# Kernel tuning notes

Hardware: AMD Instinct MI355X
Metric: run time of the kernel (lower is better)

Reference implementation:

```python
import jax, jax.numpy as jnp
import numpy as np

D_MODEL = 96
D_INNER = 2 * D_MODEL          # expand=2
D_STATE = 16
D_CONV = 4
DT_RANK = 6                    # ceil(96/16)


def setup_inputs() -> dict:
    key = jax.random.key(0)
    ks = jax.random.split(key, 12)
    B, C, H, W = 4, D_MODEL, 64, 64
    # dt_proj bias init (inverse-softplus of dt sampled log-uniform in [1e-3, 1e-1])
    dtv = jnp.exp(jax.random.uniform(ks[7], (D_INNER,), jnp.float32)
                  * (np.log(0.1) - np.log(0.001)) + np.log(0.001))
    dtv = jnp.clip(dtv, 1e-4, None)
    dt_proj_b = dtv + jnp.log(-jnp.expm1(-dtv))
    dt_std = DT_RANK ** -0.5
    return {
        "x": jax.random.normal(ks[0], (B, C, H, W), jnp.float32),
        "proj_w": jax.random.normal(ks[1], (2 * C, C, 1, 1), jnp.float32) * 0.05,
        "dconv_w": jax.random.normal(ks[2], (C, 2 * C, 3, 3), jnp.float32) * 0.02,
        "in_proj_w": jax.random.normal(ks[3], (2 * D_INNER, C), jnp.float32) * 0.05,
        "conv1d_w": jax.random.normal(ks[4], (D_INNER, D_CONV), jnp.float32) * 0.2,
        "conv1d_b": jnp.zeros((D_INNER,), jnp.float32),
        "x_proj_w": jax.random.normal(ks[5], (DT_RANK + 2 * D_STATE, D_INNER), jnp.float32) * 0.05,
        "dt_proj_w": jax.random.uniform(ks[6], (D_INNER, DT_RANK), jnp.float32, -dt_std, dt_std),
        "dt_proj_b": dt_proj_b,
        "A_log": jnp.log(jnp.tile(jnp.arange(1, D_STATE + 1, dtype=jnp.float32), (D_INNER, 1))),
        "D": jnp.ones((D_INNER,), jnp.float32),
        "out_proj_w": jax.random.normal(ks[8], (C, D_INNER), jnp.float32) * 0.05,
    }


def _cssm_forward(x, proj_w, dconv_w, in_proj_w, conv1d_w, conv1d_b,
                  x_proj_w, dt_proj_w, dt_proj_b, A_log, D, out_proj_w):
    Bsz, Cdim, H, W = x.shape
    L = H * W
    # proj (1x1 conv, no bias) then dconv (3x3 conv, pad 1, no bias)
    xp = jax.lax.conv_general_dilated(x, proj_w, (1, 1), 'VALID',
                                      dimension_numbers=('NCHW', 'OIHW', 'NCHW'))
    xp = jax.lax.conv_general_dilated(xp, dconv_w, (1, 1), ((1, 1), (1, 1)),
                                      dimension_numbers=('NCHW', 'OIHW', 'NCHW'))
    seq = xp.reshape(Bsz, Cdim, L).transpose(0, 2, 1)            # (B, L, C)
    # in_proj (no bias) -> (B, 2*d_inner, L)
    xz = jnp.einsum('blc,ec->bel', seq, in_proj_w)
    xin, z = jnp.split(xz, 2, axis=1)                             # (B, d_inner, L) each
    # causal depthwise conv1d (pad d_conv-1 on left) + SiLU
    xpad = jnp.pad(xin, ((0, 0), (0, 0), (D_CONV - 1, 0)))
    xc = jax.lax.conv_general_dilated(xpad, conv1d_w[:, None, :], (1,), 'VALID',
                                      dimension_numbers=('NCH', 'OIH', 'NCH'),
                                      feature_group_count=D_INNER)
    xc = jax.nn.silu(xc + conv1d_b[None, :, None])                # (B, d_inner, L)
    # x_proj -> dt (rank), B (state), C (state)
    x_dbl = jnp.einsum('bdl,ed->ble', xc, x_proj_w)               # (B, L, rank+2n)
    dt, Bc, Cc = jnp.split(x_dbl, [DT_RANK, DT_RANK + D_STATE], axis=-1)
    delta = jax.nn.softplus(jnp.einsum('blr,dr->bld', dt, dt_proj_w) + dt_proj_b)  # (B,L,d)
    A = -jnp.exp(A_log)                                           # (d, n)
    u = xc.transpose(0, 2, 1)                                     # (B, L, d)
    # selective scan: h_t = exp(delta_t A) * h_{t-1} + delta_t B_t u_t  (diag, per channel/state)
    dA = jnp.exp(delta[..., None] * A)                            # (B,L,d,n)
    dBu = delta[..., None] * Bc[:, :, None, :] * u[..., None]     # (B,L,d,n)

    def combine(c1, c2):
        a1, b1 = c1
        a2, b2 = c2
        return a2 * a1, a2 * b1 + b2

    _, h = jax.lax.associative_scan(combine, (dA, dBu), axis=1)   # (B,L,d,n)
    y = jnp.einsum('bldn,bln->bld', h, Cc) + D * u                # (B,L,d)
    y = y * jax.nn.silu(z.transpose(0, 2, 1))                     # gate
    out = jnp.einsum('bld,cd->blc', y, out_proj_w)                # (B,L,C)
    return out.transpose(0, 2, 1).reshape(Bsz, Cdim, H, W)


def reference(x, proj_w, dconv_w, in_proj_w, conv1d_w, conv1d_b,
              x_proj_w, dt_proj_w, dt_proj_b, A_log, D, out_proj_w):
    return _cssm_forward(x, proj_w, dconv_w, in_proj_w, conv1d_w, conv1d_b,
                         x_proj_w, dt_proj_w, dt_proj_b, A_log, D, out_proj_w)
```

## Files before the change

### kernel.cpp

```cpp
#include <hip/hip_runtime.h>
#include <math.h>

#define LL    4096
#define CDIM  96
#define DIN   192
#define NST   16
#define XE    38

typedef __attribute__((ext_vector_type(8))) short v8s;
typedef __attribute__((ext_vector_type(4))) float v4f;
typedef unsigned short ushort_t;
typedef unsigned int uint_t;

#if __has_builtin(__builtin_amdgcn_exp2f)
__device__ __forceinline__ float fexp2(float x) { return __builtin_amdgcn_exp2f(x); }
#else
__device__ __forceinline__ float fexp2(float x) { return exp2f(x); }
#endif
#if __has_builtin(__builtin_amdgcn_logf)
__device__ __forceinline__ float flog2(float x) { return __builtin_amdgcn_logf(x); }
#else
__device__ __forceinline__ float flog2(float x) { return __log2f(x); }
#endif

__device__ __forceinline__ float siluf(float x) {
    return x * __builtin_amdgcn_rcpf(1.f + fexp2(-1.44269504f * x));
}
__device__ __forceinline__ ushort_t f2bf(float f) {
    uint_t u = __builtin_bit_cast(uint_t, f);
    return (ushort_t)((u + 0x7fffu + ((u >> 16) & 1u)) >> 16);
}
__device__ __forceinline__ float bf2f(ushort_t u) {
    return __builtin_bit_cast(float, (uint_t)u << 16);
}

__global__ __launch_bounds__(256) void k_prep(const float* __restrict__ proj_w,
                                              const float* __restrict__ dconv_w,
                                              const float* __restrict__ in_proj_w,
                                              const float* __restrict__ out_proj_w,
                                              const float* __restrict__ x_proj_w,
                                              const float* __restrict__ x,
                                              ushort_t* __restrict__ Wbf,
                                              ushort_t* __restrict__ Wibf,
                                              ushort_t* __restrict__ Wobf,
                                              ushort_t* __restrict__ Wxbf,
                                              ushort_t* __restrict__ xT) {
    __shared__ float s_dc[1728];
    int bid = blockIdx.x;
    if (bid < 96) {
        int o = bid;
        for (int i = threadIdx.x; i < 1728; i += 256)
            s_dc[i] = dconv_w[o * 1728 + i];
        __syncthreads();
        for (int u2 = threadIdx.x; u2 < 864; u2 += 256) {
            int c = u2 % 96, k = u2 / 96;
            float s = 0.f;
            for (int j2 = 0; j2 < 192; ++j2)
                s = fmaf(s_dc[j2 * 9 + k], proj_w[j2 * 96 + c], s);
            Wbf[(k * 96 + o) * 96 + c] = f2bf(s);
        }
        return;
    }
    if (bid < 348) {
        int i = (bid - 96) * 256 + threadIdx.x;
        if (i < 36864) { Wibf[i] = f2bf(in_proj_w[i]); return; }
        i -= 36864;
        if (i < 18432) { Wobf[i] = f2bf(out_proj_w[i]); return; }
        i -= 18432;
        if (i < 9216) {
            int e = i / 192;
            Wxbf[i] = (e < XE) ? f2bf(x_proj_w[i]) : (ushort_t)0;
        }
        return;
    }
    int bid2 = bid - 348;
    int yy = bid2 % 66;
    int b  = bid2 / 66;
    int yv = yy - 1;
    for (int i = threadIdx.x; i < 68 * 12; i += 256) {
        int xx = i % 68, cig = i / 68;
        int xv = xx - 1;
        ushort_t u[8];
        if (yv >= 0 && yv < 64 && xv >= 0 && xv < 64) {
            const float* sp = x + ((size_t)(b * 96 + cig * 8)) * LL + yv * 64 + xv;
#pragma unroll
            for (int j = 0; j < 8; ++j) u[j] = f2bf(sp[j * LL]);
        } else {
#pragma unroll
            for (int j = 0; j < 8; ++j) u[j] = 0;
        }
        uint4 pk;
        pk.x = u[0] | ((uint_t)u[1] << 16); pk.y = u[2] | ((uint_t)u[3] << 16);
        pk.z = u[4] | ((uint_t)u[5] << 16); pk.w = u[6] | ((uint_t)u[7] << 16);
        *(uint4*)(xT + (((size_t)b * 66 + yy) * 68 + xx) * 96 + cig * 8) = pk;
    }
}

__global__ __launch_bounds__(384, 2) void k_convin(const ushort_t* __restrict__ xT,
                                                   const ushort_t* __restrict__ Wbf,
                                                   const ushort_t* __restrict__ Wibf,
                                                   ushort_t* __restrict__ xzb) {
    __shared__ ushort_t s_xt[3 * 34 * 100];
    __shared__ ushort_t s_seq[32 * 104];
    int tid = threadIdx.x;
    int w = tid >> 6, l = tid & 63;
    int n = l & 15, g = l >> 4;
    int blk = blockIdx.x;
    int b = blk >> 7, rem = blk & 127;
    int y = rem >> 1, half = rem & 1;
    int lx = (w & 1) * 16;
    int co0 = (w >> 1) * 32;
    {
        const ushort_t* gsrc = xT + ((size_t)(b * 66 + y) * 68 + half * 32) * 96;
        for (int idx = tid; idx < 1224; idx += 384) {
            int r = idx / 408, rm = idx % 408;
            int col = rm / 12, ci8 = rm % 12;
            uint4 v = *(const uint4*)(gsrc + ((size_t)r * 68 + col) * 96 + ci8 * 8);
            *(uint4*)&s_xt[(r * 34 + col) * 100 + ci8 * 8] = v;
        }
    }
    __syncthreads();
    v4f acc0 = {0.f, 0.f, 0.f, 0.f};
    v4f acc1 = {0.f, 0.f, 0.f, 0.f};
    const ushort_t* xbl = &s_xt[(lx + n) * 100 + g * 8];
    const ushort_t* aw = Wbf + ((size_t)co0 + n) * 96 + g * 8;
#pragma unroll
    for (int tap = 0; tap < 9; ++tap) {
        int dy = tap / 3, dx = tap % 3;
        const ushort_t* bp = xbl + (dy * 34 + dx) * 100;
        const ushort_t* ap = aw + (size_t)tap * 9216;
#pragma unroll
        for (int kk = 0; kk < 3; ++kk) {
            v8s bf = *(const v8s*)(bp + kk * 32);
            v8s a0 = *(const v8s*)(ap + kk * 32);
            v8s a1 = *(const v8s*)(ap + 1536 + kk * 32);
            acc0 = __builtin_amdgcn_mfma_f32_16x16x32_bf16(a0, bf, acc0, 0, 0, 0);
            acc1 = __builtin_amdgcn_mfma_f32_16x16x32_bf16(a1, bf, acc1, 0, 0, 0);
        }
    }
    {
        int ll = lx + n;
        ushort_t* sp = s_seq + ll * 104 + co0 + g * 4;
        ushort4 p0, p1;
        p0.x = f2bf(acc0[0]); p0.y = f2bf(acc0[1]); p0.z = f2bf(acc0[2]); p0.w = f2bf(acc0[3]);
        p1.x = f2bf(acc1[0]); p1.y = f2bf(acc1[1]); p1.z = f2bf(acc1[2]); p1.w = f2bf(acc1[3]);
        *(ushort4*)sp = p0;
        *(ushort4*)(sp + 16) = p1;
    }
    __syncthreads();
    int coh = w * 64;
    v4f acc[4][2];
#pragma unroll
    for (int mt = 0; mt < 4; ++mt)
#pragma unroll
        for (int lt = 0; lt < 2; ++lt) acc[mt][lt] = (v4f){0.f, 0.f, 0.f, 0.f};
    const ushort_t* ap2 = Wibf + ((size_t)coh + n) * 96 + g * 8;
#pragma unroll
    for (int lt = 0; lt < 2; ++lt) {
        const ushort_t* bp2 = s_seq + (lt * 16 + n) * 104 + g * 8;
#pragma unroll
        for (int kk = 0; kk < 3; ++kk) {
            v8s bf = *(const v8s*)(bp2 + kk * 32);
#pragma unroll
            for (int mt = 0; mt < 4; ++mt) {
                v8s af = *(const v8s*)(ap2 + mt * 16 * 96 + kk * 32);
                acc[mt][lt] = __builtin_amdgcn_mfma_f32_16x16x32_bf16(af, bf, acc[mt][lt], 0, 0, 0);
            }
        }
    }
    int l0g = y * 64 + half * 32;
    ushort_t* ob = xzb + (size_t)b * 384 * LL + l0g + n;
#pragma unroll
    for (int mt = 0; mt < 4; ++mt) {
        int e = coh + mt * 16 + g * 4;
#pragma unroll
        for (int lt = 0; lt < 2; ++lt)
#pragma unroll
            for (int r = 0; r < 4; ++r)
                ob[(size_t)(e + r) * LL + lt * 16] = f2bf(acc[mt][lt][r]);
    }
}

__global__ __launch_bounds__(256, 2) void k_convxp(const ushort_t* __restrict__ xzb,
                                                   const float* __restrict__ c1w,
                                                   const float* __restrict__ c1b,
                                                   const ushort_t* __restrict__ Wxbf,
                                                   ushort_t* __restrict__ xcR,
                                                   float* __restrict__ dtT,
                                                   float* __restrict__ BtP,
                                                   float* __restrict__ CtP) {
    __shared__ ushort_t s_xc[32][200];
    int tid = threadIdx.x;
    int b = blockIdx.y;
    int l0 = blockIdx.x * 32;
    if (tid < 192) {
        int d = tid;
        const ushort_t* xin = xzb + (size_t)(b * 384 + d) * LL;
        float e[35];
        if (l0 > 0) {
            v8s pv = *(const v8s*)(xin + l0 - 8);
            e[0] = bf2f((ushort_t)pv[5]); e[1] = bf2f((ushort_t)pv[6]); e[2] = bf2f((ushort_t)pv[7]);
        } else {
            e[0] = e[1] = e[2] = 0.f;
        }
#pragma unroll
        for (int q = 0; q < 4; ++q) {
            v8s cv = *(const v8s*)(xin + l0 + q * 8);
#pragma unroll
            for (int j = 0; j < 8; ++j) e[3 + q * 8 + j] = bf2f((ushort_t)cv[j]);
        }
        float w0 = c1w[d * 4], w1 = c1w[d * 4 + 1], w2 = c1w[d * 4 + 2], w3 = c1w[d * 4 + 3];
        float bb = c1b[d];
        ushort_t* xr = xcR + (size_t)(b * 192 + d) * LL + l0;
#pragma unroll
        for (int q = 0; q < 4; ++q) {
            v8s ov;
#pragma unroll
            for (int j = 0; j < 8; ++j) {
                int i = q * 8 + j;
                float s = bb + w0 * e[i] + w1 * e[i + 1] + w2 * e[i + 2] + w3 * e[i + 3];
                ushort_t uv = f2bf(siluf(s));
                ov[j] = (short)uv;
                s_xc[i][d] = uv;
            }
            *(v8s*)(xr + q * 8) = ov;
        }
    }
    __syncthreads();
    int w = tid >> 6, l = tid & 63;
    int n = l & 15, g = l >> 4;
    int th = w >> 1, ms = w & 1;
    int lt = th * 16;
    int t = l0 + lt + n;
    const ushort_t* ap = Wxbf + (size_t)n * 192 + g * 8;
    float* dtb = dtT + (size_t)b * 6 * LL + t;
    float* Bb  = BtP + ((size_t)b * LL + t) * 16;
    float* Cb  = CtP + ((size_t)b * LL + t) * 16;
    if (ms == 0) {
        v4f acc0 = {0.f, 0.f, 0.f, 0.f};
        v4f acc1 = {0.f, 0.f, 0.f, 0.f};
#pragma unroll
        for (int kk = 0; kk < 6; ++kk) {
            v8s bf = *(const v8s*)&s_xc[lt + n][g * 8 + kk * 32];
            v8s a0 = *(const v8s*)(ap + kk * 32);
            v8s a1 = *(const v8s*)(ap + 16 * 192 + kk * 32);
            acc0 = __builtin_amdgcn_mfma_f32_16x16x32_bf16(a0, bf, acc0, 0, 0, 0);
            acc1 = __builtin_amdgcn_mfma_f32_16x16x32_bf16(a1, bf, acc1, 0, 0, 0);
        }
#pragma unroll
        for (int r = 0; r < 4; ++r) {
            int e0 = g * 4 + r;
            float v0 = acc0[r];
            if (e0 < 6) dtb[(size_t)e0 * LL] = v0;
            else        Bb[e0 - 6] = v0;
            int e1 = 16 + g * 4 + r;
            float v1 = acc1[r];
            if (e1 < 22) Bb[e1 - 6] = v1;
            else         Cb[e1 - 22] = v1;
        }
    } else {
        v4f acc2 = {0.f, 0.f, 0.f, 0.f};
#pragma unroll
        for (int kk = 0; kk < 6; ++kk) {
            v8s bf = *(const v8s*)&s_xc[lt + n][g * 8 + kk * 32];
            v8s a2 = *(const v8s*)(ap + 2 * 16 * 192 + kk * 32);
            acc2 = __builtin_amdgcn_mfma_f32_16x16x32_bf16(a2, bf, acc2, 0, 0, 0);
        }
#pragma unroll
        for (int r = 0; r < 4; ++r) {
            int e2 = 32 + g * 4 + r;
            if (e2 < 38) Cb[e2 - 22] = acc2[r];
        }
    }
}

__global__ __launch_bounds__(512, 6) void k_scan(const float* __restrict__ dtT,
                                                 const float* __restrict__ dtw,
                                                 const float* __restrict__ dtpb,
                                                 const ushort_t* __restrict__ xcR,
                                                 const float* __restrict__ BtP,
                                                 const float* __restrict__ CtP,
                                                 const float* __restrict__ A_log,
                                                 const float* __restrict__ Dp,
                                                 ushort_t* __restrict__ xzb) {
    __shared__ float s_d[32 * 132];
    __shared__ float s_u[32 * 132];
    __shared__ float s_a[32][17];
    __shared__ float s_h[32][17];
    int tid = threadIdx.x;
    int n = tid & 15, cg = tid >> 4;
    int bd = blockIdx.x;
    int d = bd % DIN, b = bd / DIN;
    const ushort_t* urow = xcR + (size_t)(b * 192 + d) * LL;
    const ushort_t* zrow = xzb + (size_t)(b * 384 + DIN + d) * LL;
    ushort_t* ygr = xzb + (size_t)(b * 384 + d) * LL;
    float A2 = -__expf(A_log[d * NST + n]) * 1.44269504f;
    float Dd = Dp[d];

    {
        int t8 = tid * 8;
        int li = ((t8 >> 7) * 132) + (t8 & 127);
        v8s uu = *(const v8s*)(urow + t8);
        v4f u0, u1;
#pragma unroll
        for (int j = 0; j < 4; ++j) {
            u0[j] = bf2f((ushort_t)uu[j]);
            u1[j] = bf2f((ushort_t)uu[4 + j]);
        }
        *(v4f*)&s_u[li]     = u0;
        *(v4f*)&s_u[li + 4] = u1;
        const float* dt0 = dtT + (size_t)b * 6 * LL + t8;
        const float* wr = dtw + d * 6;
        float w0 = wr[0], w1 = wr[1], w2 = wr[2], w3 = wr[3], w4 = wr[4], w5 = wr[5];
        float bb = dtpb[d];
        {
            v4f ra[6];
#pragma unroll
            for (int r = 0; r < 6; ++r) ra[r] = *(const v4f*)(dt0 + r * LL);
            v4f spa;
#pragma unroll
            for (int j = 0; j < 4; ++j) {
                float s1 = bb + w0 * ra[0][j] + w1 * ra[1][j] + w2 * ra[2][j]
                              + w3 * ra[3][j] + w4 * ra[4][j] + w5 * ra[5][j];
                spa[j] = 0.69314718f * flog2(1.f + fexp2(s1 * 1.44269504f));
            }
            *(v4f*)&s_d[li] = spa;
        }
        {
            v4f rb[6];
#pragma unroll
            for (int r = 0; r < 6; ++r) rb[r] = *(const v4f*)(dt0 + r * LL + 4);
            v4f spb;
#pragma unroll
            for (int j = 0; j < 4; ++j) {
                float s2 = bb + w0 * rb[0][j] + w1 * rb[1][j] + w2 * rb[2][j]
                              + w3 * rb[3][j] + w4 * rb[4][j] + w5 * rb[5][j];
                spb[j] = 0.69314718f * flog2(1.f + fexp2(s2 * 1.44269504f));
            }
            *(v4f*)&s_d[li + 4] = spb;
        }
    }
    __syncthreads();

    int t0 = cg * 128;
    int lb = cg * 132;
    const float* pB = BtP + ((size_t)b * LL + t0) * 16 + n;
    const float* pC = CtP + ((size_t)b * LL + t0) * 16 + n;

    float h = 0.f, sdu = 0.f;
    float4 du_c = *(float4*)&s_d[lb];
    float4 u_c  = *(float4*)&s_u[lb];
    float B0 = pB[0], B1 = pB[16], B2 = pB[32], B3 = pB[48];
    for (int s = 0; s < 31; ++s) {
        int ln = lb + s * 4 + 4;
        const float* pBn = pB + s * 64 + 64;
        float4 du_n = *(float4*)&s_d[ln];
        float4 u_n  = *(float4*)&s_u[ln];
        float Bn0 = pBn[0], Bn1 = pBn[16], Bn2 = pBn[32], Bn3 = pBn[48];
        float a0 = fexp2(du_c.x * A2), a1 = fexp2(du_c.y * A2);
        float a2 = fexp2(du_c.z * A2), a3 = fexp2(du_c.w * A2);
        h = fmaf(a0, h, (du_c.x * u_c.x) * B0);
        h = fmaf(a1, h, (du_c.y * u_c.y) * B1);
        h = fmaf(a2, h, (du_c.z * u_c.z) * B2);
        h = fmaf(a3, h, (du_c.w * u_c.w) * B3);
        sdu += (du_c.x + du_c.y) + (du_c.z + du_c.w);
        du_c = du_n; u_c = u_n; B0 = Bn0; B1 = Bn1; B2 = Bn2; B3 = Bn3;
    }
    {
        float a0 = fexp2(du_c.x * A2), a1 = fexp2(du_c.y * A2);
        float a2 = fexp2(du_c.z * A2), a3 = fexp2(du_c.w * A2);
        h = fmaf(a0, h, (du_c.x * u_c.x) * B0);
        h = fmaf(a1, h, (du_c.y * u_c.y) * B1);
        h = fmaf(a2, h, (du_c.z * u_c.z) * B2);
        h = fmaf(a3, h, (du_c.w * u_c.w) * B3);
        sdu += (du_c.x + du_c.y) + (du_c.z + du_c.w);
    }
    s_a[cg][n] = fexp2(sdu * A2);
    s_h[cg][n] = h;
    __syncthreads();

    {
        int l = tid & 63, w = tid >> 6;
        int c = l & 31, nn = (w << 1) | (l >> 5);
        float a  = s_a[c][nn];
        float hh = s_h[c][nn];
#pragma unroll
        for (int st = 1; st < 32; st <<= 1) {
            float ap = __shfl_up(a, st, 32);
            float hp = __shfl_up(hh, st, 32);
            bool ok = (c >= st);
            hh = ok ? fmaf(a, hp, hh) : hh;
            a  = ok ? a * ap : a;
        }
        float h0 = __shfl_up(hh, 1, 32);
        if (c == 0) h0 = 0.f;
        s_a[c][nn] = h0;
    }
    __syncthreads();

    h = s_a[cg][n];
    const int j = n & 3;
    const bool e1 = (j == 1), e2 = (j == 2), e3 = (j == 3);
    du_c = *(float4*)&s_d[lb];
    u_c  = *(float4*)&s_u[lb];
    B0 = pB[0]; B1 = pB[16]; B2 = pB[32]; B3 = pB[48];
    float C0 = pC[0], C1 = pC[16], C2 = pC[32], C3 = pC[48];
    ushort4 z_c = *(const ushort4*)(zrow + t0);
    for (int s = 0; s < 32; ++s) {
        float4 du_n, u_n;
        ushort4 z_n;
        float Bn0, Bn1, Bn2, Bn3, Cn0, Cn1, Cn2, Cn3;
        if (s < 31) {
            int ln = lb + s * 4 + 4;
            const float* pBn = pB + s * 64 + 64;
            const float* pCn = pC + s * 64 + 64;
            du_n = *(float4*)&s_d[ln];
            u_n  = *(float4*)&s_u[ln];
            Bn0 = pBn[0]; Bn1 = pBn[16]; Bn2 = pBn[32]; Bn3 = pBn[48];
            Cn0 = pCn[0]; Cn1 = pCn[16]; Cn2 = pCn[32]; Cn3 = pCn[48];
            z_n = *(const ushort4*)(zrow + t0 + s * 4 + 4);
        }
        float a0 = fexp2(du_c.x * A2), a1 = fexp2(du_c.y * A2);
        float a2 = fexp2(du_c.z * A2), a3 = fexp2(du_c.w * A2);
        h = fmaf(a0, h, (du_c.x * u_c.x) * B0); float p0 = h * C0;
        h = fmaf(a1, h, (du_c.y * u_c.y) * B1); float p1 = h * C1;
        h = fmaf(a2, h, (du_c.z * u_c.z) * B2); float p2 = h * C2;
        h = fmaf(a3, h, (du_c.w * u_c.w) * B3); float p3 = h * C3;
        p0 += __shfl_xor(p0, 1); p0 += __shfl_xor(p0, 2);
        p1 += __shfl_xor(p1, 1); p1 += __shfl_xor(p1, 2);
        p2 += __shfl_xor(p2, 1); p2 += __shfl_xor(p2, 2);
        p3 += __shfl_xor(p3, 1); p3 += __shfl_xor(p3, 2);
        float pj = e3 ? p3 : (e2 ? p2 : (e1 ? p1 : p0));
        pj += __shfl_xor(pj, 4); pj += __shfl_xor(pj, 8);
        float uj = e3 ? u_c.w : (e2 ? u_c.z : (e1 ? u_c.y : u_c.x));
        ushort_t zu = e3 ? z_c.w : (e2 ? z_c.z : (e1 ? z_c.y : z_c.x));
        float yj = fmaf(Dd, uj, pj) * siluf(bf2f(zu));
        if (n < 4)
            ygr[t0 + s * 4 + n] = f2bf(yj);
        du_c = du_n; u_c = u_n; z_c = z_n;
        B0 = Bn0; B1 = Bn1; B2 = Bn2; B3 = Bn3;
        C0 = Cn0; C1 = Cn1; C2 = Cn2; C3 = Cn3;
    }
}

__global__ __launch_bounds__(384, 6) void k_outproj(const ushort_t* __restrict__ xzb,
                                                    const ushort_t* __restrict__ Wobf,
                                                    float* __restrict__ out) {
    __shared__ ushort_t s_yg[16][232];
    int tid = threadIdx.x;
    int b = blockIdx.y;
    int l0 = blockIdx.x * 16;
    const ushort_t* ygb = xzb + (size_t)b * 384 * LL;
    if (tid < 96) {
        int q = tid >> 1, o = tid & 1;
        uint4 v[4];
#pragma unroll
        for (int jj = 0; jj < 4; ++jj)
            v[jj] = *(const uint4*)(ygb + (size_t)(q * 4 + jj) * LL + l0 + o * 8);
        const ushort_t* vs = (const ushort_t*)v;
#pragma unroll
        for (int j2 = 0; j2 < 8; ++j2) {
            ushort4 pk;
            pk.x = vs[j2]; pk.y = vs[8 + j2]; pk.z = vs[16 + j2]; pk.w = vs[24 + j2];
            *(ushort4*)&s_yg[o * 8 + j2][q * 4] = pk;
        }
    }
    __syncthreads();
    int w = tid >> 6, l = tid & 63;
    int n = l & 15, g = l >> 4;
    int c0 = w * 16;
    const ushort_t* bp = &s_yg[n][g * 8];
    const ushort_t* ap = Wobf + ((size_t)c0 + n) * 192 + g * 8;
    v4f acc = {0.f, 0.f, 0.f, 0.f};
#pragma unroll
    for (int kk = 0; kk < 6; ++kk) {
        v8s bf = *(const v8s*)(bp + kk * 32);
        v8s af = *(const v8s*)(ap + kk * 32);
        acc = __builtin_amdgcn_mfma_f32_16x16x32_bf16(af, bf, acc, 0, 0, 0);
    }
    float* ob = out + (size_t)b * 96 * LL + l0 + n;
#pragma unroll
    for (int r = 0; r < 4; ++r)
        ob[(size_t)(c0 + g * 4 + r) * LL] = acc[r];
}

extern "C" void kernel_launch(void* const* d_in, const int* in_sizes, int n_in,
                              void* d_out, int out_size, void* d_ws, size_t ws_size,
                              hipStream_t stream) {
    const float* x         = (const float*)d_in[0];
    const float* proj_w    = (const float*)d_in[1];
    const float* dconv_w   = (const float*)d_in[2];
    const float* in_proj_w = (const float*)d_in[3];
    const float* conv1d_w  = (const float*)d_in[4];
    const float* conv1d_b  = (const float*)d_in[5];
    const float* x_proj_w  = (const float*)d_in[6];
    const float* dt_proj_w = (const float*)d_in[7];
    const float* dt_proj_b = (const float*)d_in[8];
    const float* A_log     = (const float*)d_in[9];
    const float* Dp        = (const float*)d_in[10];
    const float* out_proj_w= (const float*)d_in[11];
    float* out = (float*)d_out;
    float* ws  = (float*)d_ws;

    ushort_t* Wbf  = (ushort_t*)ws;
    ushort_t* Wibf = (ushort_t*)(ws + 41472);
    ushort_t* Wobf = (ushort_t*)(ws + 59904);
    ushort_t* Wxbf = (ushort_t*)(ws + 69120);
    ushort_t* xT   = (ushort_t*)(ws + 73728);
    ushort_t* xzb  = (ushort_t*)(ws + 1721856);
    float* dtT  = ws + 4867584;
    float* BtP  = dtT + 98304;
    float* CtP  = BtP + 262144;
    ushort_t* xcR = (ushort_t*)(CtP + 262144);

    k_prep<<<dim3(612), dim3(256), 0, stream>>>(proj_w, dconv_w, in_proj_w, out_proj_w,
                                                x_proj_w, x, Wbf, Wibf, Wobf, Wxbf, xT);
    k_convin<<<dim3(512), dim3(384), 0, stream>>>(xT, Wbf, Wibf, xzb);
    k_convxp<<<dim3(128, 4), dim3(256), 0, stream>>>(xzb, conv1d_w, conv1d_b, Wxbf,
                                                     xcR, dtT, BtP, CtP);
    k_scan<<<dim3(768), dim3(512), 0, stream>>>(dtT, dt_proj_w, dt_proj_b, xcR, BtP, CtP,
                                                A_log, Dp, xzb);
    k_outproj<<<dim3(256, 4), dim3(384), 0, stream>>>(xzb, Wobf, out);
}
```

Before: 111.9 us.

## Split selective scan into two kernels over half-sequence blocks

The single per-channel scan kernel is split into two launches, each with twice as many blocks covering half of the sequence. The first kernel computes chunk aggregates (decay product and partial state) and writes them to a global buffer. The second kernel scans all 64 chunk aggregates per state with a wave-wide prefix, then reruns the chunk scan with outputs and gating. This raises the block count and shortens each thread's serial chain, aiming to improve GPU fill and latency. The cost is recomputing softplus(dt) and the u loads twice, an extra kernel launch, a global round trip for the aggregates, and dropping the software prefetching.

```diff
diff --git a/kernel.cpp b/kernel.cpp
--- a/kernel.cpp
+++ b/kernel.cpp
@@ -274,172 +274,172 @@
     }
 }
 
-__global__ __launch_bounds__(512, 6) void k_scan(const float* __restrict__ dtT,
-                                                 const float* __restrict__ dtw,
-                                                 const float* __restrict__ dtpb,
-                                                 const ushort_t* __restrict__ xcR,
-                                                 const float* __restrict__ BtP,
-                                                 const float* __restrict__ CtP,
-                                                 const float* __restrict__ A_log,
-                                                 const float* __restrict__ Dp,
-                                                 ushort_t* __restrict__ xzb) {
-    __shared__ float s_d[32 * 132];
-    __shared__ float s_u[32 * 132];
-    __shared__ float s_a[32][17];
-    __shared__ float s_h[32][17];
+__global__ __launch_bounds__(512, 8) void k_scan1(const float* __restrict__ dtT,
+                                                  const float* __restrict__ dtw,
+                                                  const float* __restrict__ dtpb,
+                                                  const ushort_t* __restrict__ xcR,
+                                                  const float* __restrict__ BtP,
+                                                  const float* __restrict__ A_log,
+                                                  float2* __restrict__ agg) {
+    __shared__ float s_d[32 * 68];
+    __shared__ float s_u[32 * 68];
     int tid = threadIdx.x;
     int n = tid & 15, cg = tid >> 4;
-    int bd = blockIdx.x;
-    int d = bd % DIN, b = bd / DIN;
-    const ushort_t* urow = xcR + (size_t)(b * 192 + d) * LL;
-    const ushort_t* zrow = xzb + (size_t)(b * 384 + DIN + d) * LL;
-    ushort_t* ygr = xzb + (size_t)(b * 384 + d) * LL;
+    int bd2 = blockIdx.x;
+    int chain = bd2 >> 1, Hh = bd2 & 1;
+    int d = chain % DIN, b = chain / DIN;
+    int toff = Hh * 2048;
+    const ushort_t* urow = xcR + (size_t)(b * 192 + d) * LL + toff;
     float A2 = -__expf(A_log[d * NST + n]) * 1.44269504f;
-    float Dd = Dp[d];
 
     {
-        int t8 = tid * 8;
-        int li = ((t8 >> 7) * 132) + (t8 & 127);
-        v8s uu = *(const v8s*)(urow + t8);
-        v4f u0, u1;
-#pragma unroll
-        for (int j = 0; j < 4; ++j) {
-            u0[j] = bf2f((ushort_t)uu[j]);
-            u1[j] = bf2f((ushort_t)uu[4 + j]);
-        }
-        *(v4f*)&s_u[li]     = u0;
-        *(v4f*)&s_u[li + 4] = u1;
-        const float* dt0 = dtT + (size_t)b * 6 * LL + t8;
+        int t4 = tid * 4;
+        int li = (t4 >> 6) * 68 + (t4 & 63);
+        ushort4 uu = *(const ushort4*)(urow + t4);
+        v4f u0;
+        u0[0] = bf2f(uu.x); u0[1] = bf2f(uu.y); u0[2] = bf2f(uu.z); u0[3] = bf2f(uu.w);
+        *(v4f*)&s_u[li] = u0;
+        const float* dt0 = dtT + (size_t)b * 6 * LL + toff + t4;
         const float* wr = dtw + d * 6;
         float w0 = wr[0], w1 = wr[1], w2 = wr[2], w3 = wr[3], w4 = wr[4], w5 = wr[5];
         float bb = dtpb[d];
-        {
-            v4f ra[6];
-#pragma unroll
-            for (int r = 0; r < 6; ++r) ra[r] = *(const v4f*)(dt0 + r * LL);
-            v4f spa;
-#pragma unroll
-            for (int j = 0; j < 4; ++j) {
-                float s1 = bb + w0 * ra[0][j] + w1 * ra[1][j] + w2 * ra[2][j]
-                              + w3 * ra[3][j] + w4 * ra[4][j] + w5 * ra[5][j];
-                spa[j] = 0.69314718f * flog2(1.f + fexp2(s1 * 1.44269504f));
+        v4f ra[6];
+#pragma unroll
+        for (int r = 0; r < 6; ++r) ra[r] = *(const v4f*)(dt0 + r * LL);
+        v4f spa;
+#pragma unroll
+        for (int j = 0; j < 4; ++j) {
+            float s1 = bb + w0 * ra[0][j] + w1 * ra[1][j] + w2 * ra[2][j]
+                          + w3 * ra[3][j] + w4 * ra[4][j] + w5 * ra[5][j];
+            spa[j] = 0.69314718f * flog2(1.f + fexp2(s1 * 1.44269504f));
+        }
+        *(v4f*)&s_d[li] = spa;
+    }
+    __syncthreads();
+
+    int lb = cg * 68;
+    const float* pB = BtP + ((size_t)b * LL + toff + cg * 64) * 16 + n;
+    float h = 0.f, sdu = 0.f;
+    for (int s = 0; s < 16; ++s) {
+        const float* pBs = pB + s * 64;
+        float4 du = *(float4*)&s_d[lb + s * 4];
+        float4 uc = *(float4*)&s_u[lb + s * 4];
+        float B0 = pBs[0], B1 = pBs[16], B2 = pBs[32], B3 = pBs[48];
+        float a0 = fexp2(du.x * A2), a1 = fexp2(du.y * A2);
+        float a2 = fexp2(du.z * A2), a3 = fexp2(du.w * A2);
+        h = fmaf(a0, h, (du.x * uc.x) * B0);
+        h = fmaf(a1, h, (du.y * uc.y) * B1);
+        h = fmaf(a2, h, (du.z * uc.z) * B2);
+        h = fmaf(a3, h, (du.w * uc.w) * B3);
+        sdu += (du.x + du.y) + (du.z + du.w);
+    }
+    float2 ag; ag.x = fexp2(sdu * A2); ag.y = h;
+    agg[((size_t)chain * NST + n) * 64 + Hh * 32 + cg] = ag;
+}
+
+__global__ __launch_bounds__(512, 8) void k_scan2(const float* __restrict__ dtT,
+                                                  const float* __restrict__ dtw,
+                                                  const float* __restrict__ dtpb,
+                                                  const ushort_t* __restrict__ xcR,
+                                                  const float* __restrict__ BtP,
+                                                  const float* __restrict__ CtP,
+                                                  const float* __restrict__ A_log,
+                                                  const float* __restrict__ Dp,
+                                                  const float2* __restrict__ agg,
+                                                  ushort_t* __restrict__ xzb) {
+    __shared__ float s_d[32 * 68];
+    __shared__ float s_u[32 * 68];
+    __shared__ float s_h0[64][17];
+    int tid = threadIdx.x;
+    int n = tid & 15, cg = tid >> 4;
+    int bd2 = blockIdx.x;
+    int chain = bd2 >> 1, Hh = bd2 & 1;
+    int d = chain % DIN, b = chain / DIN;
+    int toff = Hh * 2048;
+    const ushort_t* urow = xcR + (size_t)(b * 192 + d) * LL + toff;
+    const ushort_t* zrow = xzb + (size_t)(b * 384 + DIN + d) * LL + toff;
+    ushort_t* ygr = xzb + (size_t)(b * 384 + d) * LL + toff;
+    float A2 = -__expf(A_log[d * NST + n]) * 1.44269504f;
+    float Dd = Dp[d];
+
+    {
+        int t4 = tid * 4;
+        int li = (t4 >> 6) * 68 + (t4 & 63);
+        ushort4 uu = *(const ushort4*)(urow + t4);
+        v4f u0;
+        u0[0] = bf2f(uu.x); u0[1] = bf2f(uu.y); u0[2] = bf2f(uu.z); u0[3] = bf2f(uu.w);
+        *(v4f*)&s_u[li] = u0;
+        const float* dt0 = dtT + (size_t)b * 6 * LL + toff + t4;
+        const float* wr = dtw + d * 6;
+        float w0 = wr[0], w1 = wr[1], w2 = wr[2], w3 = wr[3], w4 = wr[4], w5 = wr[5];
+        float bb = dtpb[d];
+        v4f ra[6];
+#pragma unroll
+        for (int r = 0; r < 6; ++r) ra[r] = *(const v4f*)(dt0 + r * LL);
+        v4f spa;
+#pragma unroll
+        for (int j = 0; j < 4; ++j) {
+            float s1 = bb + w0 * ra[0][j] + w1 * ra[1][j] + w2 * ra[2][j]
+                          + w3 * ra[3][j] + w4 * ra[4][j] + w5 * ra[5][j];
+            spa[j] = 0.69314718f * flog2(1.f + fexp2(s1 * 1.44269504f));
+        }
+        *(v4f*)&s_d[li] = spa;
+    }
+    {
+        int lane = tid & 63, wv = tid >> 6;
+        const float2* ac = agg + (size_t)chain * NST * 64;
+#pragma unroll
+        for (int q = 0; q < 2; ++q) {
+            int n2 = wv * 2 + q;
+            float2 ag = ac[(size_t)n2 * 64 + lane];
+            float a = ag.x, hh = ag.y;
+#pragma unroll
+            for (int st = 1; st < 64; st <<= 1) {
+                float ap = __shfl_up(a, st);
+                float hp = __shfl_up(hh, st);
+                bool ok = (lane >= st);
+                hh = ok ? fmaf(a, hp, hh) : hh;
+                a  = ok ? a * ap : a;
             }
-            *(v4f*)&s_d[li] = spa;
-        }
-        {
-            v4f rb[6];
-#pragma unroll
-            for (int r = 0; r < 6; ++r) rb[r] = *(const v4f*)(dt0 + r * LL + 4);
-            v4f spb;
-#pragma unroll
-            for (int j = 0; j < 4; ++j) {
-                float s2 = bb + w0 * rb[0][j] + w1 * rb[1][j] + w2 * rb[2][j]
-                              + w3 * rb[3][j] + w4 * rb[4][j] + w5 * rb[5][j];
-                spb[j] = 0.69314718f * flog2(1.f + fexp2(s2 * 1.44269504f));
-            }
-            *(v4f*)&s_d[li + 4] = spb;
+            float h0 = __shfl_up(hh, 1);
+            if (lane == 0) h0 = 0.f;
+            s_h0[lane][n2] = h0;
         }
     }
     __syncthreads();
 
-    int t0 = cg * 128;
-    int lb = cg * 132;
-    const float* pB = BtP + ((size_t)b * LL + t0) * 16 + n;
-    const float* pC = CtP + ((size_t)b * LL + t0) * 16 + n;
-
-    float h = 0.f, sdu = 0.f;
-    float4 du_c = *(float4*)&s_d[lb];
-    float4 u_c  = *(float4*)&s_u[lb];
-    float B0 = pB[0], B1 = pB[16], B2 = pB[32], B3 = pB[48];
-    for (int s = 0; s < 31; ++s) {
-        int ln = lb + s * 4 + 4;
-        const float* pBn = pB + s * 64 + 64;
-        float4 du_n = *(float4*)&s_d[ln];
-        float4 u_n  = *(float4*)&s_u[ln];
-        float Bn0 = pBn[0], Bn1 = pBn[16], Bn2 = pBn[32], Bn3 = pBn[48];
-        float a0 = fexp2(du_c.x * A2), a1 = fexp2(du_c.y * A2);
-        float a2 = fexp2(du_c.z * A2), a3 = fexp2(du_c.w * A2);
-        h = fmaf(a0, h, (du_c.x * u_c.x) * B0);
-        h = fmaf(a1, h, (du_c.y * u_c.y) * B1);
-        h = fmaf(a2, h, (du_c.z * u_c.z) * B2);
-        h = fmaf(a3, h, (du_c.w * u_c.w) * B3);
-        sdu += (du_c.x + du_c.y) + (du_c.z + du_c.w);
-        du_c = du_n; u_c = u_n; B0 = Bn0; B1 = Bn1; B2 = Bn2; B3 = Bn3;
-    }
-    {
-        float a0 = fexp2(du_c.x * A2), a1 = fexp2(du_c.y * A2);
-        float a2 = fexp2(du_c.z * A2), a3 = fexp2(du_c.w * A2);
-        h = fmaf(a0, h, (du_c.x * u_c.x) * B0);
-        h = fmaf(a1, h, (du_c.y * u_c.y) * B1);
-        h = fmaf(a2, h, (du_c.z * u_c.z) * B2);
-        h = fmaf(a3, h, (du_c.w * u_c.w) * B3);
-        sdu += (du_c.x + du_c.y) + (du_c.z + du_c.w);
-    }
-    s_a[cg][n] = fexp2(sdu * A2);
-    s_h[cg][n] = h;
-    __syncthreads();
-
-    {
-        int l = tid & 63, w = tid >> 6;
-        int c = l & 31, nn = (w << 1) | (l >> 5);
-        float a  = s_a[c][nn];
-        float hh = s_h[c][nn];
-#pragma unroll
-        for (int st = 1; st < 32; st <<= 1) {
-            float ap = __shfl_up(a, st, 32);
-            float hp = __shfl_up(hh, st, 32);
-            bool ok = (c >= st);
-            hh = ok ? fmaf(a, hp, hh) : hh;
-            a  = ok ? a * ap : a;
-        }
-        float h0 = __shfl_up(hh, 1, 32);
-        if (c == 0) h0 = 0.f;
-        s_a[c][nn] = h0;
-    }
-    __syncthreads();
-
-    h = s_a[cg][n];
+    int lb = cg * 68;
+    int t0l = cg * 64;
+    const float* pB = BtP + ((size_t)b * LL + toff + t0l) * 16 + n;
+    const float* pC = CtP + ((size_t)b * LL + toff + t0l) * 16 + n;
+    float h = s_h0[Hh * 32 + cg][n];
     const int j = n & 3;
     const bool e1 = (j == 1), e2 = (j == 2), e3 = (j == 3);
-    du_c = *(float4*)&s_d[lb];
-    u_c  = *(float4*)&s_u[lb];
-    B0 = pB[0]; B1 = pB[16]; B2 = pB[32]; B3 = pB[48];
-    float C0 = pC[0], C1 = pC[16], C2 = pC[32], C3 = pC[48];
-    ushort4 z_c = *(const ushort4*)(zrow + t0);
-    for (int s = 0; s < 32; ++s) {
-        float4 du_n, u_n;
-        ushort4 z_n;
-        float Bn0, Bn1, Bn2, Bn3, Cn0, Cn1, Cn2, Cn3;
-        if (s < 31) {
-            int ln = lb + s * 4 + 4;
-            const float* pBn = pB + s * 64 + 64;
-            const float* pCn = pC + s * 64 + 64;
-            du_n = *(float4*)&s_d[ln];
-            u_n  = *(float4*)&s_u[ln];
-            Bn0 = pBn[0]; Bn1 = pBn[16]; Bn2 = pBn[32]; Bn3 = pBn[48];
-            Cn0 = pCn[0]; Cn1 = pCn[16]; Cn2 = pCn[32]; Cn3 = pCn[48];
-            z_n = *(const ushort4*)(zrow + t0 + s * 4 + 4);
-        }
-        float a0 = fexp2(du_c.x * A2), a1 = fexp2(du_c.y * A2);
-        float a2 = fexp2(du_c.z * A2), a3 = fexp2(du_c.w * A2);
-        h = fmaf(a0, h, (du_c.x * u_c.x) * B0); float p0 = h * C0;
-        h = fmaf(a1, h, (du_c.y * u_c.y) * B1); float p1 = h * C1;
-        h = fmaf(a2, h, (du_c.z * u_c.z) * B2); float p2 = h * C2;
-        h = fmaf(a3, h, (du_c.w * u_c.w) * B3); float p3 = h * C3;
+    for (int s = 0; s < 16; ++s) {
+        const float* pBs = pB + s * 64;
+        const float* pCs = pC + s * 64;
+        float4 du = *(float4*)&s_d[lb + s * 4];
+        float4 uc = *(float4*)&s_u[lb + s * 4];
+        float B0 = pBs[0], B1 = pBs[16], B2 = pBs[32], B3 = pBs[48];
+        float C0 = pCs[0], C1 = pCs[16], C2 = pCs[32], C3 = pCs[48];
+        ushort4 zc = *(const ushort4*)(zrow + t0l + s * 4);
+        float a0 = fexp2(du.x * A2), a1 = fexp2(du.y * A2);
+        float a2 = fexp2(du.z * A2), a3 = fexp2(du.w * A2);
+        h = fmaf(a0, h, (du.x * uc.x) * B0); float p0 = h * C0;
+        h = fmaf(a1, h, (du.y * uc.y) * B1); float p1 = h * C1;
+        h = fmaf(a2, h, (du.z * uc.z) * B2); float p2 = h * C2;
+        h = fmaf(a3, h, (du.w * uc.w) * B3); float p3 = h * C3;
         p0 += __shfl_xor(p0, 1); p0 += __shfl_xor(p0, 2);
         p1 += __shfl_xor(p1, 1); p1 += __shfl_xor(p1, 2);
         p2 += __shfl_xor(p2, 1); p2 += __shfl_xor(p2, 2);
         p3 += __shfl_xor(p3, 1); p3 += __shfl_xor(p3, 2);
         float pj = e3 ? p3 : (e2 ? p2 : (e1 ? p1 : p0));
         pj += __shfl_xor(pj, 4); pj += __shfl_xor(pj, 8);
-        float uj = e3 ? u_c.w : (e2 ? u_c.z : (e1 ? u_c.y : u_c.x));
-        ushort_t zu = e3 ? z_c.w : (e2 ? z_c.z : (e1 ? z_c.y : z_c.x));
+        float uj = e3 ? uc.w : (e2 ? uc.z : (e1 ? uc.y : uc.x));
+        ushort_t zu = e3 ? zc.w : (e2 ? zc.z : (e1 ? zc.y : zc.x));
         float yj = fmaf(Dd, uj, pj) * siluf(bf2f(zu));
         if (n < 4)
-            ygr[t0 + s * 4 + n] = f2bf(yj);
-        du_c = du_n; u_c = u_n; z_c = z_n;
-        B0 = Bn0; B1 = Bn1; B2 = Bn2; B3 = Bn3;
-        C0 = Cn0; C1 = Cn1; C2 = Cn2; C3 = Cn3;
+            ygr[t0l + s * 4 + n] = f2bf(yj);
     }
 }
 
@@ -512,13 +512,16 @@
     float* BtP  = dtT + 98304;
     float* CtP  = BtP + 262144;
     ushort_t* xcR = (ushort_t*)(CtP + 262144);
+    float2* agg = (float2*)(CtP + 262144 + 1572864);
 
     k_prep<<<dim3(612), dim3(256), 0, stream>>>(proj_w, dconv_w, in_proj_w, out_proj_w,
                                                 x_proj_w, x, Wbf, Wibf, Wobf, Wxbf, xT);
     k_convin<<<dim3(512), dim3(384), 0, stream>>>(xT, Wbf, Wibf, xzb);
     k_convxp<<<dim3(128, 4), dim3(256), 0, stream>>>(xzb, conv1d_w, conv1d_b, Wxbf,
                                                      xcR, dtT, BtP, CtP);
-    k_scan<<<dim3(768), dim3(512), 0, stream>>>(dtT, dt_proj_w, dt_proj_b, xcR, BtP, CtP,
-                                                A_log, Dp, xzb);
+    k_scan1<<<dim3(1536), dim3(512), 0, stream>>>(dtT, dt_proj_w, dt_proj_b, xcR, BtP,
+                                                  A_log, agg);
+    k_scan2<<<dim3(1536), dim3(512), 0, stream>>>(dtT, dt_proj_w, dt_proj_b, xcR, BtP, CtP,
+                                                  A_log, Dp, agg, xzb);
     k_outproj<<<dim3(256, 4), dim3(384), 0, stream>>>(xzb, Wobf, out);
 }
```

Result: no change. 113.8 us (+1.7%).
